# Optimization experiments

Measured on AMD Instinct MI355X. Metric: run time of the kernel, lower is better.

## Reference

```python
import jax, jax.numpy as jnp
import numpy as np

GRID = 128
DIMS = [64 + 3, 128, 64, 32, 1]  # MLP channel stack from source


def setup_inputs() -> dict:
    key = jax.random.key(0)
    ks = jax.random.split(key, 1 + 2 * (len(DIMS) - 1))
    B = 1
    inp = {"x": jax.random.normal(ks[0], (B, 64, 1, 1), dtype=jnp.float32)}
    for i in range(len(DIMS) - 1):
        cin, cout = DIMS[i], DIMS[i + 1]
        scale = 1.0 / np.sqrt(cin)
        inp[f"W{i+1}"] = jax.random.uniform(ks[1 + 2 * i], (cout, cin), jnp.float32, -scale, scale)
        inp[f"b{i+1}"] = jax.random.uniform(ks[2 + 2 * i], (cout,), jnp.float32, -scale, scale)
    return inp


def _forward(x, W1, b1, W2, b2, W3, b3, W4, b4):
    B = x.shape[0]
    dt = x.dtype
    lines = jnp.linspace(-1.0, 1.0, GRID, dtype=dt)
    a, b, c = jnp.meshgrid(lines, lines, lines, indexing="ij")  # torch default 'ij'
    pts = jnp.stack([a, b, c], axis=0).reshape(3, -1)           # [3, N], N = 128^3
    N = pts.shape[1]
    # broadcast latent over all grid points and concat coords -> [B, 67, N]
    f = jnp.concatenate(
        [jnp.broadcast_to(x.reshape(B, 64, 1), (B, 64, N)),
         jnp.broadcast_to(pts[None], (B, 3, N))],
        axis=1,
    )
    h = jax.nn.relu(jnp.einsum("oc,bcn->bon", W1, f) + b1[:, None])
    h = jax.nn.relu(jnp.einsum("oc,bcn->bon", W2, h) + b2[:, None])
    h = jax.nn.relu(jnp.einsum("oc,bcn->bon", W3, h) + b3[:, None])
    sdf = jax.nn.sigmoid(jnp.einsum("oc,bcn->bon", W4, h) + b4[:, None])  # [B,1,N]
    return sdf.reshape(B, GRID, GRID, GRID)


def reference(x, W1, b1, W2, b2, W3, b3, W4, b4):
    return _forward(x, W1, b1, W2, b2, W3, b3, W4, b4)
```

## Files before the change

kernel.cpp:

```cpp
#include <hip/hip_runtime.h>
#include <hip/hip_bf16.h>
#include <hip/hip_fp16.h>


#define NPTS (128 * 128 * 128)

typedef float f32x4_t __attribute__((ext_vector_type(4)));
typedef float f32x2_t __attribute__((ext_vector_type(2)));
typedef __fp16 g16x2_t __attribute__((ext_vector_type(2)));
typedef _Float16 h16x8_t __attribute__((ext_vector_type(8)));
typedef unsigned u32x2_t __attribute__((ext_vector_type(2)));

__device__ __forceinline__ unsigned h2u(g16x2_t h) {
    unsigned u;
    __builtin_memcpy(&u, &h, 4);
    return u;
}
__device__ __forceinline__ g16x2_t u2h(unsigned u) {
    g16x2_t h;
    __builtin_memcpy(&h, &u, 4);
    return h;
}

__device__ __forceinline__ void pl32_swap(unsigned& a, unsigned& b) {
#if __has_builtin(__builtin_amdgcn_permlane32_swap)
    u32x2_t r = __builtin_amdgcn_permlane32_swap(a, b, false, false);
    a = r[0];
    b = r[1];
#else
    asm("v_permlane32_swap_b32 %0, %1" : "+v"(a), "+v"(b));
#endif
}
__device__ __forceinline__ void pl16_swap(unsigned& a, unsigned& b) {
#if __has_builtin(__builtin_amdgcn_permlane16_swap)
    u32x2_t r = __builtin_amdgcn_permlane16_swap(a, b, false, false);
    a = r[0];
    b = r[1];
#else
    asm("v_permlane16_swap_b32 %0, %1" : "+v"(a), "+v"(b));
#endif
}

__global__ __launch_bounds__(256, 2) void mlp_kernel(
    const float* __restrict__ x,  const float* __restrict__ W1,
    const float* __restrict__ b1, const float* __restrict__ W2,
    const float* __restrict__ b2, const float* __restrict__ W3,
    const float* __restrict__ b3, const float* __restrict__ W4,
    const float* __restrict__ b4, float* __restrict__ out) {
    __shared__ __align__(16) unsigned s_basep[16][64];
    __shared__ __align__(16) unsigned s_wcp[64];
    __shared__ __align__(16) float s_b2[64];
    __shared__ __align__(16) float s_b3[32];
    __shared__ __align__(16) float s_w4[32];
    __shared__ __align__(16) unsigned short s_u[11264];

    const int t = threadIdx.x;
    const int w = t >> 6;
    const int lane = t & 63;
    const int quad = lane >> 4;
    const int l15 = lane & 15;
    const float step = 2.0f / 127.0f;

    {
        const int p = t & 63, h = t >> 6;
        const float* r0 = W1 + (2 * p) * 67 + h * 16;
        const float* r1 = r0 + 67;
        const float* xh = x + h * 16;
        float s0 = 0.0f, s1 = 0.0f;
#pragma unroll
        for (int c = 0; c < 16; ++c) {
            const float xc = xh[c];
            s0 = fmaf(r0[c], xc, s0);
            s1 = fmaf(r1[c], xc, s1);
        }
        float2* psum = (float2*)&s_u[10240];
        psum[h * 64 + p] = make_float2(s0, s1);
    }
    const float2* W2v = (const float2*)W2;
#pragma unroll
    for (int it = 0; it < 16; ++it) {
        int pidx = t + 256 * it;
        int idx2 = pidx * 2;
        int o = idx2 >> 7, k = idx2 & 127;
        int mt = o >> 4, lm = o & 15;
        int kb = k >> 5, q = (k >> 3) & 3, jj = k & 7;
        float2 v = W2v[pidx];
        *(unsigned*)&s_u[(mt * 4 + kb) * 512 + (q * 16 + lm) * 8 + jj] =
            h2u(__builtin_amdgcn_cvt_pkrtz(v.x, v.y));
    }
    const float2* W3v = (const float2*)W3;
#pragma unroll
    for (int it = 0; it < 4; ++it) {
        int pidx = t + 256 * it;
        int idx2 = pidx * 2;
        int o = idx2 >> 6, k = idx2 & 63;
        int mt = o >> 4, lm = o & 15;
        int kb = k >> 5, q = (k >> 3) & 3, jj = k & 7;
        float2 v = W3v[pidx];
        *(unsigned*)&s_u[8192 + (mt * 2 + kb) * 512 + (q * 16 + lm) * 8 + jj] =
            h2u(__builtin_amdgcn_cvt_pkrtz(v.x, v.y));
    }
    if (t < 64) s_b2[t] = b2[t];
    if (t < 32) {
        s_b3[t] = b3[t];
        s_w4[t] = W4[t];
    }
    const float bias4 = b4[0];
    __syncthreads();

    if (t < 64) {
        const float2* psum = (const float2*)&s_u[10240];
        float2 q0 = psum[t], q1 = psum[64 + t], q2 = psum[128 + t], q3 = psum[192 + t];
        float s0 = b1[2 * t] + (q0.x + q1.x) + (q2.x + q3.x);
        float s1 = b1[2 * t + 1] + (q0.y + q1.y) + (q2.y + q3.y);
        const float* r0 = W1 + (2 * t) * 67;
        const float* r1 = r0 + 67;
        const float pa = -1.0f + step * (float)(blockIdx.x >> 3);
        const float base0 = fmaf(r0[64], pa, s0);
        const float base1 = fmaf(r1[64], pa, s1);
        const float wb0 = r0[65], wb1 = r1[65];
        const int gj0 = (blockIdx.x & 7) * 16;
        s_wcp[t] = h2u(__builtin_amdgcn_cvt_pkrtz(r0[66], r1[66]));
#pragma unroll
        for (int j = 0; j < 16; ++j) {
            const float pb = -1.0f + step * (float)(gj0 + j);
            s_basep[j][t] = h2u(__builtin_amdgcn_cvt_pkrtz(
                fmaf(wb0, pb, base0), fmaf(wb1, pb, base1)));
        }
    }
    __syncthreads();

    h16x8_t a2[16];
#pragma unroll
    for (int f = 0; f < 16; ++f) a2[f] = *(const h16x8_t*)&s_u[f * 512 + lane * 8];
    h16x8_t a3[4];
#pragma unroll
    for (int f = 0; f < 4; ++f) a3[f] = *(const h16x8_t*)&s_u[8192 + f * 512 + lane * 8];
    f32x4_t b2q[4];
#pragma unroll
    for (int mt = 0; mt < 4; ++mt) b2q[mt] = *(const f32x4_t*)&s_b2[mt * 16 + quad * 4];
    f32x4_t b3q[2];
    f32x2_t w4lo[2], w4hi[2];
#pragma unroll
    for (int mt = 0; mt < 2; ++mt) {
        b3q[mt] = *(const f32x4_t*)&s_b3[mt * 16 + quad * 4];
        float4 wq = *(const float4*)&s_w4[mt * 16 + quad * 4];
        w4lo[mt][0] = wq.x; w4lo[mt][1] = wq.y;
        w4hi[mt][0] = wq.z; w4hi[mt][1] = wq.w;
    }
    unsigned twp[16];
#pragma unroll
    for (int kb = 0; kb < 4; ++kb) {
        uint4 v = *(const uint4*)&s_wcp[kb * 16 + quad * 4];
        twp[kb * 4 + 0] = v.x; twp[kb * 4 + 1] = v.y;
        twp[kb * 4 + 2] = v.z; twp[kb * 4 + 3] = v.w;
    }
#pragma unroll
    for (int i = 0; i < 16; ++i) asm volatile("" : "+v"(twp[i]));

    const f32x2_t zero2 = {0.0f, 0.0f};
    const g16x2_t zero2h = {(__fp16)0.0f, (__fp16)0.0f};
    const int outbase = blockIdx.x * 2048 + w * 512;

    for (int jrow = 0; jrow < 4; ++jrow) {
        const unsigned* bp = &s_basep[w * 4 + jrow][0];
        unsigned tbp[16];
#pragma unroll
        for (int kb = 0; kb < 4; ++kb) {
            uint4 v = *(const uint4*)&bp[kb * 16 + quad * 4];
            tbp[kb * 4 + 0] = v.x; tbp[kb * 4 + 1] = v.y;
            tbp[kb * 4 + 2] = v.z; tbp[kb * 4 + 3] = v.w;
        }
#pragma unroll
        for (int i = 0; i < 16; ++i) asm volatile("" : "+v"(tbp[i]));

#pragma unroll 2
        for (int pg = 0; pg < 8; ++pg) {
            const int ng = jrow * 8 + pg;
            const float pc = fmaf(step, (float)((pg * 16) + l15), -1.0f);
            const g16x2_t pc2 = __builtin_amdgcn_cvt_pkrtz(pc, pc);

            h16x8_t bfrag[4];
#pragma unroll
            for (int kb = 0; kb < 4; ++kb) {
                union { h16x8_t v; g16x2_t h[4]; } bb;
#pragma unroll
                for (int p = 0; p < 4; ++p) {
                    g16x2_t hh = __builtin_elementwise_fma(
                        u2h(twp[kb * 4 + p]), pc2, u2h(tbp[kb * 4 + p]));
                    bb.h[p] = __builtin_elementwise_max(hh, zero2h);
                }
                bfrag[kb] = bb.v;
            }
            f32x4_t acc2[4];
#pragma unroll
            for (int mt = 0; mt < 4; ++mt) {
                f32x4_t c = b2q[mt];
#pragma unroll
                for (int kb = 0; kb < 4; ++kb)
                    c = __builtin_amdgcn_mfma_f32_16x16x32_f16(a2[mt * 4 + kb], bfrag[kb], c, 0, 0, 0);
                acc2[mt] = c;
            }
            unsigned u[4][2];
#pragma unroll
            for (int mt = 0; mt < 4; ++mt) {
                u[mt][0] = h2u(__builtin_elementwise_max(
                    __builtin_amdgcn_cvt_pkrtz(acc2[mt][0], acc2[mt][1]), zero2h));
                u[mt][1] = h2u(__builtin_elementwise_max(
                    __builtin_amdgcn_cvt_pkrtz(acc2[mt][2], acc2[mt][3]), zero2h));
            }
            h16x8_t b3f[2];
#pragma unroll
            for (int kb = 0; kb < 2; ++kb) {
                union { h16x8_t v; unsigned wd[4]; } fb;
#pragma unroll
                for (int s = 0; s < 2; ++s) {
                    unsigned A = u[2 * kb][s], B = u[2 * kb + 1][s];
                    pl32_swap(A, B);
                    pl16_swap(A, B);
                    fb.wd[s] = A;
                    fb.wd[2 + s] = B;
                }
                b3f[kb] = fb.v;
            }
            f32x2_t z2 = zero2;
#pragma unroll
            for (int mt = 0; mt < 2; ++mt) {
                f32x4_t c = b3q[mt];
                c = __builtin_amdgcn_mfma_f32_16x16x32_f16(a3[mt * 2 + 0], b3f[0], c, 0, 0, 0);
                c = __builtin_amdgcn_mfma_f32_16x16x32_f16(a3[mt * 2 + 1], b3f[1], c, 0, 0, 0);
                f32x2_t h01 = __builtin_elementwise_max((f32x2_t){c[0], c[1]}, zero2);
                f32x2_t h23 = __builtin_elementwise_max((f32x2_t){c[2], c[3]}, zero2);
                z2 = __builtin_elementwise_fma(w4lo[mt], h01, z2);
                z2 = __builtin_elementwise_fma(w4hi[mt], h23, z2);
            }
            float z = z2[0] + z2[1];
            unsigned za = __builtin_bit_cast(unsigned, z), zb = za;
            pl16_swap(za, zb);
            z = __builtin_bit_cast(float, za) + __builtin_bit_cast(float, zb);
            za = __builtin_bit_cast(unsigned, z); zb = za;
            pl32_swap(za, zb);
            z = __builtin_bit_cast(float, za) + __builtin_bit_cast(float, zb) + bias4;
            const float r = 1.0f / (1.0f + __expf(-z));
            if (quad == 0) out[outbase + ng * 16 + l15] = r;
        }
    }
}

extern "C" void kernel_launch(void* const* d_in, const int* in_sizes, int n_in,
                              void* d_out, int out_size, void* d_ws, size_t ws_size,
                              hipStream_t stream) {
    mlp_kernel<<<NPTS / 2048, 256, 0, stream>>>(
        (const float*)d_in[0], (const float*)d_in[1], (const float*)d_in[2],
        (const float*)d_in[3], (const float*)d_in[4], (const float*)d_in[5],
        (const float*)d_in[6], (const float*)d_in[7], (const float*)d_in[8],
        (float*)d_out);
}
```

Measured before the change: 116.2 us.

## Software-pipeline layer-3/4 phase one point-group behind layer-2 MFMAs

Splits the per-group work so the layer-3/4 MFMA, reduction and sigmoid for group ng-1 run after the layer-2 MFMAs of group ng. Packed layer-2 activations are carried across iterations and a final epilogue handles the last group. The aim is to hide MFMA latency and the cross-lane permute dependency chains by interleaving independent work. In exchange it raises register pressure and makes the loop structure more complex.

```diff
diff --git a/kernel.cpp b/kernel.cpp
--- a/kernel.cpp
+++ b/kernel.cpp
@@ -162,6 +162,48 @@
     const g16x2_t zero2h = {(__fp16)0.0f, (__fp16)0.0f};
     const int outbase = blockIdx.x * 2048 + w * 512;
 
+    auto bphase = [&](unsigned pu00, unsigned pu01, unsigned pu10, unsigned pu11,
+                      unsigned pu20, unsigned pu21, unsigned pu30, unsigned pu31,
+                      int ngp) {
+        h16x8_t b3f[2];
+        {
+            union { h16x8_t v; unsigned wd[4]; } fb;
+            unsigned A, B;
+            A = pu00; B = pu10; pl32_swap(A, B); pl16_swap(A, B);
+            fb.wd[0] = A; fb.wd[2] = B;
+            A = pu01; B = pu11; pl32_swap(A, B); pl16_swap(A, B);
+            fb.wd[1] = A; fb.wd[3] = B;
+            b3f[0] = fb.v;
+            A = pu20; B = pu30; pl32_swap(A, B); pl16_swap(A, B);
+            fb.wd[0] = A; fb.wd[2] = B;
+            A = pu21; B = pu31; pl32_swap(A, B); pl16_swap(A, B);
+            fb.wd[1] = A; fb.wd[3] = B;
+            b3f[1] = fb.v;
+        }
+        f32x2_t z2 = zero2;
+#pragma unroll
+        for (int mt = 0; mt < 2; ++mt) {
+            f32x4_t c = b3q[mt];
+            c = __builtin_amdgcn_mfma_f32_16x16x32_f16(a3[mt * 2 + 0], b3f[0], c, 0, 0, 0);
+            c = __builtin_amdgcn_mfma_f32_16x16x32_f16(a3[mt * 2 + 1], b3f[1], c, 0, 0, 0);
+            f32x2_t h01 = __builtin_elementwise_max((f32x2_t){c[0], c[1]}, zero2);
+            f32x2_t h23 = __builtin_elementwise_max((f32x2_t){c[2], c[3]}, zero2);
+            z2 = __builtin_elementwise_fma(w4lo[mt], h01, z2);
+            z2 = __builtin_elementwise_fma(w4hi[mt], h23, z2);
+        }
+        float z = z2[0] + z2[1];
+        unsigned za = __builtin_bit_cast(unsigned, z), zb = za;
+        pl16_swap(za, zb);
+        z = __builtin_bit_cast(float, za) + __builtin_bit_cast(float, zb);
+        za = __builtin_bit_cast(unsigned, z); zb = za;
+        pl32_swap(za, zb);
+        z = __builtin_bit_cast(float, za) + __builtin_bit_cast(float, zb) + bias4;
+        const float r = 1.0f / (1.0f + __expf(-z));
+        if (quad == 0) out[outbase + ngp * 16 + l15] = r;
+    };
+
+    unsigned pu[4][2];
+
     for (int jrow = 0; jrow < 4; ++jrow) {
         const unsigned* bp = &s_basep[w * 4 + jrow][0];
         unsigned tbp[16];
@@ -201,50 +243,21 @@
                     c = __builtin_amdgcn_mfma_f32_16x16x32_f16(a2[mt * 4 + kb], bfrag[kb], c, 0, 0, 0);
                 acc2[mt] = c;
             }
-            unsigned u[4][2];
+            if (ng > 0) {
+                bphase(pu[0][0], pu[0][1], pu[1][0], pu[1][1],
+                       pu[2][0], pu[2][1], pu[3][0], pu[3][1], ng - 1);
+            }
 #pragma unroll
             for (int mt = 0; mt < 4; ++mt) {
-                u[mt][0] = h2u(__builtin_elementwise_max(
+                pu[mt][0] = h2u(__builtin_elementwise_max(
                     __builtin_amdgcn_cvt_pkrtz(acc2[mt][0], acc2[mt][1]), zero2h));
-                u[mt][1] = h2u(__builtin_elementwise_max(
+                pu[mt][1] = h2u(__builtin_elementwise_max(
                     __builtin_amdgcn_cvt_pkrtz(acc2[mt][2], acc2[mt][3]), zero2h));
             }
-            h16x8_t b3f[2];
-#pragma unroll
-            for (int kb = 0; kb < 2; ++kb) {
-                union { h16x8_t v; unsigned wd[4]; } fb;
-#pragma unroll
-                for (int s = 0; s < 2; ++s) {
-                    unsigned A = u[2 * kb][s], B = u[2 * kb + 1][s];
-                    pl32_swap(A, B);
-                    pl16_swap(A, B);
-                    fb.wd[s] = A;
-                    fb.wd[2 + s] = B;
-                }
-                b3f[kb] = fb.v;
-            }
-            f32x2_t z2 = zero2;
-#pragma unroll
-            for (int mt = 0; mt < 2; ++mt) {
-                f32x4_t c = b3q[mt];
-                c = __builtin_amdgcn_mfma_f32_16x16x32_f16(a3[mt * 2 + 0], b3f[0], c, 0, 0, 0);
-                c = __builtin_amdgcn_mfma_f32_16x16x32_f16(a3[mt * 2 + 1], b3f[1], c, 0, 0, 0);
-                f32x2_t h01 = __builtin_elementwise_max((f32x2_t){c[0], c[1]}, zero2);
-                f32x2_t h23 = __builtin_elementwise_max((f32x2_t){c[2], c[3]}, zero2);
-                z2 = __builtin_elementwise_fma(w4lo[mt], h01, z2);
-                z2 = __builtin_elementwise_fma(w4hi[mt], h23, z2);
-            }
-            float z = z2[0] + z2[1];
-            unsigned za = __builtin_bit_cast(unsigned, z), zb = za;
-            pl16_swap(za, zb);
-            z = __builtin_bit_cast(float, za) + __builtin_bit_cast(float, zb);
-            za = __builtin_bit_cast(unsigned, z); zb = za;
-            pl32_swap(za, zb);
-            z = __builtin_bit_cast(float, za) + __builtin_bit_cast(float, zb) + bias4;
-            const float r = 1.0f / (1.0f + __expf(-z));
-            if (quad == 0) out[outbase + ng * 16 + l15] = r;
-        }
-    }
+        }
+    }
+    bphase(pu[0][0], pu[0][1], pu[1][0], pu[1][1],
+           pu[2][0], pu[2][1], pu[3][0], pu[3][1], 31);
 }
 
 extern "C" void kernel_launch(void* const* d_in, const int* in_sizes, int n_in,
```

Result: no change. 117.5 us (+1.1%).
